# Performance work log

Measured on AMD Instinct MI355X. Metric: run time of the kernel, lower is better.

Reference implementation:

```python
import jax, jax.numpy as jnp
import numpy as np

EMB = 1024
HEADS = 16
FFN = 4096
EPS = 1e-5


def _layernorm(x, g, b):
    mu = jnp.mean(x, axis=-1, keepdims=True)
    var = jnp.mean((x - mu) ** 2, axis=-1, keepdims=True)
    return (x - mu) * jax.lax.rsqrt(var + EPS) * g + b


def setup_inputs() -> dict:
    key = jax.random.key(0)
    ks = jax.random.split(key, 8)
    B, T = 2, 2048
    s_in = 1.0 / np.sqrt(EMB)
    s_ffn = 1.0 / np.sqrt(FFN)
    return {
        "x": jax.random.normal(ks[0], (B, T, EMB), jnp.float32),
        "positions": jnp.arange(B * T, dtype=jnp.int64 if jax.config.jax_enable_x64 else jnp.int32).reshape(B, T),
        "ln1_g": jnp.ones((EMB,), jnp.float32),
        "ln1_b": jnp.zeros((EMB,), jnp.float32),
        "ln2_g": jnp.ones((EMB,), jnp.float32),
        "ln2_b": jnp.zeros((EMB,), jnp.float32),
        "Wq": jax.random.normal(ks[1], (EMB, EMB), jnp.float32) * s_in,
        "bq": jnp.zeros((EMB,), jnp.float32),
        "Wk": jax.random.normal(ks[2], (EMB, EMB), jnp.float32) * s_in,
        "bk": jnp.zeros((EMB,), jnp.float32),
        "Wv": jax.random.normal(ks[3], (EMB, EMB), jnp.float32) * s_in,
        "bv": jnp.zeros((EMB,), jnp.float32),
        "Wo": jax.random.normal(ks[4], (EMB, EMB), jnp.float32) * s_in,
        "bo": jnp.zeros((EMB,), jnp.float32),
        "W1": jax.random.normal(ks[5], (EMB, FFN), jnp.float32) * s_in,
        "b1": jnp.zeros((FFN,), jnp.float32),
        "W2": jax.random.normal(ks[6], (FFN, EMB), jnp.float32) * s_ffn,
        "b2": jnp.zeros((EMB,), jnp.float32),
    }


def reference(x, positions, ln1_g, ln1_b, ln2_g, ln2_b,
              Wq, bq, Wk, bk, Wv, bv, Wo, bo, W1, b1, W2, b2):
    B, T, C = x.shape
    H, D = HEADS, C // HEADS
    # x = ln1(x); then residual branches add onto the normalized x (as in source)
    x = _layernorm(x, ln1_g, ln1_b)
    # --- self attention (rope=None, mask=None, dropout inactive) ---
    q = (x @ Wq + bq).reshape(B, T, H, D).transpose(0, 2, 1, 3)  # [B,H,T,D]
    k = (x @ Wk + bk).reshape(B, T, H, D).transpose(0, 2, 1, 3)
    v = (x @ Wv + bv).reshape(B, T, H, D).transpose(0, 2, 1, 3)
    scale = 1.0 / jnp.sqrt(jnp.asarray(D, x.dtype))
    attn = jnp.einsum("bhtd,bhsd->bhts", q, k) * scale  # [B,H,T,T]
    attn = jax.nn.softmax(attn, axis=-1)
    attn_out = jnp.einsum("bhts,bhsd->bhtd", attn, v)
    attn_out = attn_out.transpose(0, 2, 1, 3).reshape(B, T, C)
    attn_out = attn_out @ Wo + bo
    x = x + attn_out
    # --- FFN with exact (erf) GELU, matching torch nn.GELU default ---
    h = _layernorm(x, ln2_g, ln2_b)
    h = jax.nn.gelu(h @ W1 + b1, approximate=False)
    h = h @ W2 + b2
    return x + h
```

## Files before the change

kernel.cpp:

```cpp
#include <hip/hip_runtime.h>
#include <cstdint>
#include <cstddef>

typedef __bf16 bf16;
typedef __bf16 bf16x8 __attribute__((ext_vector_type(8)));
typedef __bf16 bf16x4 __attribute__((ext_vector_type(4)));
typedef float f32x4 __attribute__((ext_vector_type(4)));
typedef float f32x16 __attribute__((ext_vector_type(16)));

#define TOKENS 4096
#define TSEQ   2048
#define NHEADS 16
#define HDIM   64
#define CDIM   1024

typedef __attribute__((address_space(3))) unsigned int lds_uint;
typedef __attribute__((address_space(1))) const unsigned int g_uint;
__device__ __forceinline__ void glds16(const bf16* g, bf16* l) {
  __builtin_amdgcn_global_load_lds((g_uint*)g, (lds_uint*)l, 16, 0, 0);
}

__device__ __forceinline__ float gelu_f(float v) {
  float g2 = v * (1.5957691216f + 0.0713548163f * v * v);
  return v / (1.0f + __expf(-g2));
}

#define NBUF 17
struct DetectArgs { const void* p[NBUF]; int n[NBUF]; };

__global__ __launch_bounds__(256) void detect_kernel(DetectArgs a, int* __restrict__ flags) {
  __shared__ int s_nz, s_bl;
  if (threadIdx.x == 0) { s_nz = 0; s_bl = 0; }
  __syncthreads();
  int i = blockIdx.x;
  const unsigned int* w = (const unsigned int*)a.p[i];
  int nwords = a.n[i] / 2; if (nwords > 2048) nwords = 2048;
  int nz = 0, bl = 0;
  for (int j = threadIdx.x; j < nwords; j += 256) {
    unsigned int v = w[j];
    if (v != 0u) {
      nz++;
      unsigned int e = (v >> 7) & 0xFFu;
      if (e >= 100u && e <= 140u) bl++;
    }
  }
  atomicAdd(&s_nz, nz);
  atomicAdd(&s_bl, bl);
  __syncthreads();
  if (threadIdx.x == 0) flags[i] = (2 * s_bl >= s_nz) ? 1 : 0;
}

__device__ __forceinline__ float ld_any(const void* p, size_t idx, bool isb) {
  return isb ? (float)((const bf16*)p)[idx] : ((const float*)p)[idx];
}

__device__ __forceinline__ void ln_stats(float s, float s2, int tid, float& mu, float& rstd) {
#pragma unroll
  for (int off = 32; off; off >>= 1) {
    s  += __shfl_down(s, off);
    s2 += __shfl_down(s2, off);
  }
  __shared__ float red[8];
  int w = tid >> 6;
  if ((tid & 63) == 0) { red[w] = s; red[4 + w] = s2; }
  __syncthreads();
  if (tid == 0) {
    red[0] = red[0] + red[1] + red[2] + red[3];
    red[4] = red[4] + red[5] + red[6] + red[7];
  }
  __syncthreads();
  mu = red[0] * (1.0f / CDIM);
  float var = fmaxf(red[4] * (1.0f / CDIM) - mu * mu, 0.f);
  rstd = rsqrtf(var + 1e-5f);
}

__global__ __launch_bounds__(256) void ln_f32(const float* __restrict__ x,
                                              const bf16* __restrict__ g,
                                              const bf16* __restrict__ b,
                                              bf16* __restrict__ y) {
  int row = blockIdx.x, tid = threadIdx.x;
  float v[4]; float s = 0.f, s2 = 0.f;
#pragma unroll
  for (int i = 0; i < 4; i++) {
    float f = x[(size_t)row * CDIM + tid * 4 + i];
    v[i] = f; s += f; s2 += f * f;
  }
  float mu, rstd;
  ln_stats(s, s2, tid, mu, rstd);
  bf16* yr = y + (size_t)row * CDIM;
#pragma unroll
  for (int i = 0; i < 4; i++) {
    int c = tid * 4 + i;
    yr[c] = (bf16)((v[i] - mu) * rstd * (float)g[c] + (float)b[c]);
  }
}

struct MegaArgs {
  const void* w_in[6]; bf16* w_out[6]; int wK[6], wN[6], wflag[6];
  const void* vp[10]; bf16* vd[10]; int vn[10], vfi[10];
  const void* x; const void* graw; const void* braw; bf16* y;
};

__global__ __launch_bounds__(256) void mega_pre(MegaArgs a, const int* __restrict__ flags) {
  int bid = blockIdx.x;
  int tx = threadIdx.x, ty = threadIdx.y;
  int tid = tx + ty * 64;
  if (bid < 3072) {
    __shared__ bf16 tile[64][65];
    int mi, start;
    if (bid < 1024)      { mi = bid >> 8; start = mi << 8; }
    else if (bid < 2048) { mi = 4; start = 1024; }
    else                 { mi = 5; start = 2048; }
    int tb = bid - start;
    int nT = a.wN[mi] >> 6;
    int kb = (tb / nT) * 64, nb = (tb % nT) * 64;
    int K = a.wK[mi], N = a.wN[mi];
    bool isb = flags[a.wflag[mi]] != 0;
    const void* in = a.w_in[mi]; bf16* out = a.w_out[mi];
    for (int i = ty; i < 64; i += 4)
      tile[i][tx] = (bf16)ld_any(in, (size_t)(kb + i) * N + nb + tx, isb);
    __syncthreads();
    for (int i = ty; i < 64; i += 4)
      out[(size_t)(nb + i) * K + kb + tx] = tile[tx][i];
  } else if (bid == 3072) {
    for (int i = 0; i < 10; i++) {
      bool isb = flags[a.vfi[i]] != 0;
      const void* in = a.vp[i]; bf16* out = a.vd[i]; int n = a.vn[i];
      for (int j = tid; j < n; j += 256)
        out[j] = (bf16)ld_any(in, j, isb);
    }
  } else {
    int row = bid - 3073;
    bool isb  = flags[0] != 0;
    bool gisb = flags[1] != 0;
    bool bisb = flags[2] != 0;
    float v[4]; float s = 0.f, s2 = 0.f;
#pragma unroll
    for (int i = 0; i < 4; i++) {
      float f = ld_any(a.x, (size_t)row * CDIM + tid * 4 + i, isb);
      v[i] = f; s += f; s2 += f * f;
    }
    float mu, rstd;
    ln_stats(s, s2, tid, mu, rstd);
    bf16* yr = a.y + (size_t)row * CDIM;
#pragma unroll
    for (int i = 0; i < 4; i++) {
      int c = tid * 4 + i;
      float gv = ld_any(a.graw, c, gisb);
      float bv = ld_any(a.braw, c, bisb);
      yr[c] = (bf16)((v[i] - mu) * rstd * gv + bv);
    }
  }
}

template <int BM, int BN>
__device__ __forceinline__ void gemm_core(const bf16* __restrict__ A,
                                          const bf16* __restrict__ Bt,
                                          int K, int m0, int n0,
                                          bf16* As, bf16* Bs,
                                          f32x4 (&acc)[BM / 32][BN / 32]) {
  constexpr int SI = BM / 32, SJ = BN / 32;
  int t = threadIdx.x;
  int wave = t >> 6, lane = t & 63, quad = lane >> 4, l16 = lane & 15;
  int wm = (wave & 1) * (BM / 2), wn = (wave >> 1) * (BN / 2);
  int srow = t >> 2, sc = t & 3;
  int swz = (srow >> 1) & 3;
  const bf16* ga[BM / 64];
  const bf16* gb[BN / 64];
#pragma unroll
  for (int h = 0; h < BM / 64; h++)
    ga[h] = A + (size_t)(m0 + h * 64 + srow) * K + (sc ^ swz) * 8;
#pragma unroll
  for (int h = 0; h < BN / 64; h++)
    gb[h] = Bt + (size_t)(n0 + h * 64 + srow) * K + (sc ^ swz) * 8;

  for (int k0 = 0; k0 < K; k0 += 64) {
#pragma unroll
    for (int q = 0; q < 2; q++) {
#pragma unroll
      for (int h = 0; h < BM / 64; h++)
        glds16(ga[h] + k0 + q * 32, As + q * (BM * 32) + h * 2048 + srow * 32 + sc * 8);
#pragma unroll
      for (int h = 0; h < BN / 64; h++)
        glds16(gb[h] + k0 + q * 32, Bs + q * (BN * 32) + h * 2048 + srow * 32 + sc * 8);
    }
    __syncthreads();
#pragma unroll
    for (int q = 0; q < 2; q++) {
      bf16x8 af[SI], bfr[SJ];
#pragma unroll
      for (int i = 0; i < SI; i++) {
        int m = wm + i * 16 + l16;
        af[i] = *(const bf16x8*)&As[q * (BM * 32) + m * 32 + ((quad ^ ((m >> 1) & 3)) * 8)];
      }
#pragma unroll
      for (int j = 0; j < SJ; j++) {
        int n = wn + j * 16 + l16;
        bfr[j] = *(const bf16x8*)&Bs[q * (BN * 32) + n * 32 + ((quad ^ ((n >> 1) & 3)) * 8)];
      }
#pragma unroll
      for (int i = 0; i < SI; i++)
#pragma unroll
        for (int j = 0; j < SJ; j++)
          acc[i][j] = __builtin_amdgcn_mfma_f32_16x16x32_bf16(af[i], bfr[j], acc[i][j], 0, 0, 0);
    }
    __syncthreads();
  }
}

#define EPI_NONE 0
#define EPI_RES  1
#define EPI_GELU 2

template <int BM, int BN, int EPI, typename OutT, typename ResT>
__global__ __launch_bounds__(256) void gemm128(const bf16* __restrict__ A,
                                               const bf16* __restrict__ Bt,
                                               const bf16* __restrict__ bias,
                                               const ResT* __restrict__ res,
                                               OutT* __restrict__ C,
                                               int N, int K) {
  __shared__ alignas(16) bf16 As[2 * BM * 32];
  __shared__ alignas(16) bf16 Bs[2 * BN * 32];
  int m0 = blockIdx.y * BM, n0 = blockIdx.x * BN;
  f32x4 acc[BM / 32][BN / 32] = {};
  gemm_core<BM, BN>(A, Bt, K, m0, n0, As, Bs, acc);

  int t = threadIdx.x, wave = t >> 6, lane = t & 63, quad = lane >> 4, l16 = lane & 15;
  int wm = (wave & 1) * (BM / 2), wn = (wave >> 1) * (BN / 2);
#pragma unroll
  for (int i = 0; i < BM / 32; i++)
#pragma unroll
    for (int j = 0; j < BN / 32; j++) {
      int n = n0 + wn + j * 16 + l16;
      float bv = (float)bias[n];
#pragma unroll
      for (int r = 0; r < 4; r++) {
        int m = m0 + wm + i * 16 + quad * 4 + r;
        float v = acc[i][j][r] + bv;
        if (EPI == EPI_GELU)      v = gelu_f(v);
        else if (EPI == EPI_RES)  v += (float)res[(size_t)m * N + n];
        C[(size_t)m * N + n] = (OutT)v;
      }
    }
}

__device__ __forceinline__ void gemm256_core(const bf16* __restrict__ A,
                                             const bf16* __restrict__ Bt,
                                             int K, int m0, int n0,
                                             bf16* sm, f32x4 (&acc)[8][4]) {
  const int NT = K >> 6;
  const int t = threadIdx.x;
  const int lane = t & 63, quad = lane >> 4, l16 = lane & 15;
  const int wave = t >> 6;
  const int wm = (wave & 1) * 128, wn = (wave >> 1) * 64;
  const int srow = t >> 2, sc = t & 3;
  const int swz = (srow >> 1) & 3;
  const int rA = (srow & 63) + ((srow >> 6) << 7);
  const bf16* gA = A + (size_t)(m0 + rA) * K + ((sc ^ swz) << 3);
  const bf16* gB = Bt + (size_t)(n0 + srow) * K + ((sc ^ swz) << 3);
  const int ldsA = rA * 32 + sc * 8;
  const int ldsB = srow * 32 + sc * 8;

  auto stA = [&](int tile, int u) {
    if (tile >= NT) return;
    const bf16* g = gA + (size_t)(u << 6) * K + (tile << 6);
    bf16* l = sm + ((tile & 1) << 15) + ldsA + (u << 11);
    glds16(g, l);
    glds16(g + 32, l + 8192);
  };
  auto stB = [&](int tile, int h) {
    if (tile >= NT) return;
    const bf16* g = gB + (size_t)(h << 7) * K + (tile << 6);
    bf16* l = sm + ((tile & 1) << 15) + 16384 + ldsB + (h << 12);
    glds16(g, l);
    glds16(g + 32, l + 8192);
  };

  stB(0, 0); stB(0, 1); stA(0, 0); stA(0, 1);
  stB(1, 0); stB(1, 1); stA(1, 0);
  asm volatile("s_waitcnt vmcnt(6)" ::: "memory");
  __builtin_amdgcn_s_barrier();
  asm volatile("" ::: "memory");

  bf16x8 bfr[2][4];

#define LDB256(buf)                                                        \
  _Pragma("unroll") for (int q = 0; q < 2; q++)                            \
  _Pragma("unroll") for (int j = 0; j < 4; j++) {                          \
    int nl = wn + j * 16 + l16;                                            \
    bfr[q][j] = *(const bf16x8*)&sm[((buf) << 15) + 16384 + q * 8192 +     \
                                    nl * 32 + ((quad ^ ((nl >> 1) & 3)) << 3)]; \
  }

#define PHASE256(buf, P, STAGE, EXTRAWAIT)                                 \
  {                                                                        \
    bf16x8 af[2][2];                                                       \
    _Pragma("unroll") for (int q = 0; q < 2; q++)                          \
    _Pragma("unroll") for (int i2 = 0; i2 < 2; i2++) {                     \
      int ml = wm + (P) * 32 + i2 * 16 + l16;                              \
      af[q][i2] = *(const bf16x8*)&sm[((buf) << 15) + q * 8192 + ml * 32 + \
                                      ((quad ^ ((ml >> 1) & 3)) << 3)];    \
    }                                                                      \
    if ((P) == 0) { LDB256(buf); }                                         \
    STAGE;                                                                 \
    asm volatile("" ::: "memory");                                         \
    __builtin_amdgcn_s_barrier();                                          \
    asm volatile("s_waitcnt lgkmcnt(0)" ::: "memory");                     \
    __builtin_amdgcn_s_setprio(1);                                         \
    _Pragma("unroll") for (int q = 0; q < 2; q++)                          \
    _Pragma("unroll") for (int i2 = 0; i2 < 2; i2++)                       \
    _Pragma("unroll") for (int j = 0; j < 4; j++)                          \
      acc[(P) * 2 + i2][j] = __builtin_amdgcn_mfma_f32_16x16x32_bf16(      \
          af[q][i2], bfr[q][j], acc[(P) * 2 + i2][j], 0, 0, 0);            \
    __builtin_amdgcn_s_setprio(0);                                         \
    asm volatile("" ::: "memory");                                         \
    EXTRAWAIT;                                                             \
    __builtin_amdgcn_s_barrier();                                          \
    asm volatile("" ::: "memory");                                         \
  }

  for (int t0 = 0; t0 < NT; t0 += 2) {
    const int t1 = t0 + 1;
    PHASE256(0, 0, stA(t1, 1), (void)0);
    PHASE256(0, 1, stB(t0 + 2, 0), (void)0);
    PHASE256(0, 2, stB(t0 + 2, 1), (void)0);
    PHASE256(0, 3, stA(t0 + 2, 0),
             asm volatile("s_waitcnt vmcnt(6)" ::: "memory"));
    PHASE256(1, 0, stA(t0 + 2, 1), (void)0);
    PHASE256(1, 1, stB(t1 + 2, 0), (void)0);
    PHASE256(1, 2, stB(t1 + 2, 1), (void)0);
    PHASE256(1, 3, stA(t1 + 2, 0),
             asm volatile("s_waitcnt vmcnt(6)" ::: "memory"));
  }
#undef PHASE256
#undef LDB256
}

__device__ __forceinline__ void xcd_swizzle(int& bx, int& by) {
  int gx = gridDim.x;
  int nwg = gx * gridDim.y;
  int bid = blockIdx.x + blockIdx.y * gx;
  int wg = (bid & 7) * (nwg >> 3) + (bid >> 3);
  bx = wg % gx; by = wg / gx;
}

__global__ __launch_bounds__(512, 2) void gemm256_gelu(const bf16* __restrict__ A,
                                                       const bf16* __restrict__ Bt,
                                                       const bf16* __restrict__ bias,
                                                       bf16* __restrict__ C,
                                                       int N, int K) {
  __shared__ alignas(16) bf16 sm[65536];
  int bx, by; xcd_swizzle(bx, by);
  int m0 = by * 256, n0 = bx * 256;
  f32x4 acc[8][4] = {};
  gemm256_core(A, Bt, K, m0, n0, sm, acc);

  int t = threadIdx.x, wave = t >> 6, lane = t & 63, quad = lane >> 4, l16 = lane & 15;
  int wm = (wave & 1) * 128, wn = (wave >> 1) * 64;
#pragma unroll
  for (int i = 0; i < 8; i++)
#pragma unroll
    for (int j = 0; j < 4; j++) {
      int n = n0 + wn + j * 16 + l16;
      float bv = (float)bias[n];
#pragma unroll
      for (int r = 0; r < 4; r++) {
        int m = m0 + wm + i * 16 + quad * 4 + r;
        C[(size_t)m * N + n] = (bf16)gelu_f(acc[i][j][r] + bv);
      }
    }
}

__global__ __launch_bounds__(512, 2) void gemm256_qkv(const bf16* __restrict__ A,
                                                      const bf16* __restrict__ Bt,
                                                      const bf16* __restrict__ bias,
                                                      bf16* __restrict__ QK,
                                                      bf16* __restrict__ Vt) {
  __shared__ alignas(16) bf16 sm[65536];
  int bx, by; xcd_swizzle(bx, by);
  int m0 = by * 256, n0 = bx * 256;
  f32x4 acc[8][4] = {};
  gemm256_core(A, Bt, 1024, m0, n0, sm, acc);

  int t = threadIdx.x, wave = t >> 6, lane = t & 63, quad = lane >> 4, l16 = lane & 15;
  int wm = (wave & 1) * 128, wn = (wave >> 1) * 64;
#pragma unroll
  for (int i = 0; i < 8; i++)
#pragma unroll
    for (int j = 0; j < 4; j++) {
      int n = n0 + wn + j * 16 + l16;
      float bv = (float)bias[n];
      int mb = m0 + wm + i * 16 + quad * 4;
      if (n < 1024) {
#pragma unroll
        for (int r = 0; r < 4; r++)
          QK[(size_t)(mb + r) * 2048 + n] = (bf16)((acc[i][j][r] + bv) * 0.18033688011112042f);
      } else if (n < 2048) {
#pragma unroll
        for (int r = 0; r < 4; r++)
          QK[(size_t)(mb + r) * 2048 + n] = (bf16)(acc[i][j][r] + bv);
      } else {
        bf16x4 pk;
#pragma unroll
        for (int r = 0; r < 4; r++) pk[r] = (bf16)(acc[i][j][r] + bv);
        *(bf16x4*)&Vt[(size_t)(n - 2048) * TOKENS + mb] = pk;
      }
    }
}

__global__ __launch_bounds__(256, 2) void attn_kernel(const bf16* __restrict__ QK,
                                                      const bf16* __restrict__ Vt,
                                                      bf16* __restrict__ O) {
  __shared__ alignas(16) bf16 Ks[2][4096];
  __shared__ alignas(16) bf16 Vs[2][4096];
  __shared__ alignas(16) bf16 Ps[4][2048];
  int b = blockIdx.z, h = blockIdx.y, q0 = blockIdx.x * 128;
  int t = threadIdx.x, wave = t >> 6, lane = t & 63;
  int l31 = lane & 31, l5 = lane >> 5, l7 = lane & 7;

  const bf16* Qg = QK;
  const bf16* Kg = QK + 1024;
  const size_t bT = (size_t)b * TSEQ;
  const int h64 = h * 64;

  int sr = lane >> 3;
  int sch = l7 ^ sr;
  auto stage = [&](int tile, int buf) {
    size_t krow = bT + tile * 64 + wave * 8 + sr;
    bf16* kd = &Ks[buf][wave * 512 + lane * 8];
    glds16(&Kg[krow * 2048 + h64 + sch * 8], kd);
    glds16(&Kg[(krow + 32) * 2048 + h64 + sch * 8], kd + 2048);
    size_t vrow = (size_t)(h64 + wave * 8 + sr) * TOKENS + bT + tile * 64 + sch * 8;
    bf16* vd = &Vs[buf][wave * 512 + lane * 8];
    glds16(&Vt[vrow], vd);
    glds16(&Vt[vrow + (size_t)32 * TOKENS], vd + 2048);
  };

  bf16x8 qf[4];
  {
    size_t qrow = bT + q0 + wave * 32 + l31;
    const bf16* qp = &Qg[qrow * 2048 + h64 + l5 * 8];
#pragma unroll
    for (int ds = 0; ds < 4; ds++) qf[ds] = *(const bf16x8*)(qp + ds * 16);
  }

  bf16* PW = &Ps[wave][0];
  int qb = 4 * l5, c0 = l31 >> 3;
  int pwb[8];
#pragma unroll
  for (int kvt = 0; kvt < 2; kvt++)
#pragma unroll
    for (int r3 = 0; r3 < 4; r3++)
      pwb[kvt * 4 + r3] = (qb + r3) * 64 + (((kvt * 4 + c0) ^ (r3 + qb)) * 8) + l7;

  f32x16 accO0 = {}, accO1 = {}, accL = {};
  const bf16 one = (bf16)1.0f;
  const bf16x8 onesv = {one, one, one, one, one, one, one, one};

  stage(0, 0);
  __syncthreads();

  for (int it = 0; it < TSEQ / 64; it++) {
    int cur = it & 1;
    if (it + 1 < TSEQ / 64) stage(it + 1, cur ^ 1);

    const bf16* KsC = &Ks[cur][0];
    const bf16* VsC = &Vs[cur][0];

    f32x16 st0 = {}, st1 = {};
#pragma unroll
    for (int ds = 0; ds < 4; ds++) {
      int chs = ((ds * 2 + l5) ^ l7) * 8;
      bf16x8 k0 = *(const bf16x8*)&KsC[l31 * 64 + chs];
      bf16x8 k1 = *(const bf16x8*)&KsC[(32 + l31) * 64 + chs];
      st0 = __builtin_amdgcn_mfma_f32_32x32x16_bf16(qf[ds], k0, st0, 0, 0, 0);
      st1 = __builtin_amdgcn_mfma_f32_32x32x16_bf16(qf[ds], k1, st1, 0, 0, 0);
    }

#pragma unroll
    for (int r = 0; r < 16; r++)
      PW[pwb[r & 3] + (r >> 2) * 512] = (bf16)exp2f(fminf(st0[r], 86.f));
#pragma unroll
    for (int r = 0; r < 16; r++)
      PW[pwb[4 + (r & 3)] + (r >> 2) * 512] = (bf16)exp2f(fminf(st1[r], 86.f));

    bf16x8 pa[4];
#pragma unroll
    for (int ks = 0; ks < 4; ks++)
      pa[ks] = *(const bf16x8*)&PW[l31 * 64 + (((ks * 2 + l5) ^ l7) * 8)];

#pragma unroll
    for (int ks = 0; ks < 4; ks++) {
      int chs = ((ks * 2 + l5) ^ l7) * 8;
      bf16x8 v0 = *(const bf16x8*)&VsC[l31 * 64 + chs];
      bf16x8 v1 = *(const bf16x8*)&VsC[(32 + l31) * 64 + chs];
      accO0 = __builtin_amdgcn_mfma_f32_32x32x16_bf16(pa[ks], v0, accO0, 0, 0, 0);
      accO1 = __builtin_amdgcn_mfma_f32_32x32x16_bf16(pa[ks], v1, accO1, 0, 0, 0);
      accL  = __builtin_amdgcn_mfma_f32_32x32x16_bf16(pa[ks], onesv, accL, 0, 0, 0);
    }

    __syncthreads();
  }

#pragma unroll
  for (int r = 0; r < 16; r++) {
    int q = (r & 3) + 8 * (r >> 2) + 4 * l5;
    float rl = 1.0f / fmaxf(accL[r], 1e-30f);
    size_t orow = (bT + q0 + wave * 32 + q) * CDIM + h64;
    O[orow + l31]      = (bf16)(accO0[r] * rl);
    O[orow + 32 + l31] = (bf16)(accO1[r] * rl);
  }
}

extern "C" void kernel_launch(void* const* d_in, const int* in_sizes, int n_in,
                              void* d_out, int out_size, void* d_ws, size_t ws_size,
                              hipStream_t stream) {
  char* ws = (char*)d_ws;
  const size_t MB = 1024 * 1024;
  const size_t KB = 1024;

  int* flags = (int*)ws;
  bf16* vec_c = (bf16*)(ws + 4 * KB);
  bf16* ln1g_c = vec_c + 0 * 8192;
  bf16* ln1b_c = vec_c + 1 * 8192;
  bf16* ln2g_c = vec_c + 2 * 8192;
  bf16* ln2b_c = vec_c + 3 * 8192;
  bf16* bqkv_c = vec_c + 4 * 8192;
  bf16* bo_c   = vec_c + 6 * 8192;
  bf16* b1_c   = vec_c + 7 * 8192;
  bf16* b2_c   = vec_c + 8 * 8192;

  bf16*  WqkvT  = (bf16*)(ws + 1 * MB);
  bf16*  WoT    = (bf16*)(ws + 7 * MB);
  bf16*  W1T    = (bf16*)(ws + 9 * MB);
  bf16*  W2T    = (bf16*)(ws + 17 * MB);
  bf16*  xn     = (bf16*)(ws + 25 * MB);
  bf16*  QKbuf  = (bf16*)(ws + 33 * MB);
  bf16*  Vtbuf  = (bf16*)(ws + 49 * MB);
  bf16*  ab     = (bf16*)(ws + 57 * MB);
  float* xmid32 = (float*)(ws + 65 * MB);
  bf16*  h2     = (bf16*)(ws + 81 * MB);
  bf16*  f1     = (bf16*)(ws + 33 * MB);

  const int din_idx[NBUF] = {0, 2, 3, 4, 5, 6, 7, 8, 9, 10, 11, 12, 13, 14, 15, 16, 17};
  DetectArgs da;
  for (int i = 0; i < NBUF; i++) { da.p[i] = d_in[din_idx[i]]; da.n[i] = in_sizes[din_idx[i]]; }
  detect_kernel<<<NBUF, 256, 0, stream>>>(da, flags);

  MegaArgs ma;
  {
    const void* wi[6] = {d_in[6], d_in[8], d_in[10], d_in[12], d_in[14], d_in[16]};
    bf16* wo[6] = {WqkvT, WqkvT + 1024 * 1024, WqkvT + 2 * 1024 * 1024, WoT, W1T, W2T};
    const int wK[6] = {1024, 1024, 1024, 1024, 1024, 4096};
    const int wN[6] = {1024, 1024, 1024, 1024, 4096, 1024};
    const int wf[6] = {5, 7, 9, 11, 13, 15};
    for (int i = 0; i < 6; i++) {
      ma.w_in[i] = wi[i]; ma.w_out[i] = wo[i];
      ma.wK[i] = wK[i]; ma.wN[i] = wN[i]; ma.wflag[i] = wf[i];
    }
    const int vf[10] = {1, 2, 3, 4, 6, 8, 10, 12, 14, 16};
    bf16* vd[10] = {ln1g_c, ln1b_c, ln2g_c, ln2b_c,
                    bqkv_c, bqkv_c + 1024, bqkv_c + 2048, bo_c, b1_c, b2_c};
    for (int i = 0; i < 10; i++) {
      int di = din_idx[vf[i]];
      ma.vp[i] = d_in[di]; ma.vd[i] = vd[i]; ma.vn[i] = in_sizes[di]; ma.vfi[i] = vf[i];
    }
    ma.x = d_in[0]; ma.graw = d_in[2]; ma.braw = d_in[3]; ma.y = xn;
  }
  mega_pre<<<3072 + 1 + TOKENS, dim3(64, 4), 0, stream>>>(ma, flags);

  gemm256_qkv<<<dim3(12, 16), 512, 0, stream>>>(xn, WqkvT, bqkv_c, QKbuf, Vtbuf);

  attn_kernel<<<dim3(TSEQ / 128, NHEADS, 2), 256, 0, stream>>>(QKbuf, Vtbuf, ab);

  gemm128<64, 128, EPI_RES, float, bf16><<<dim3(8, 64), 256, 0, stream>>>(
      ab, WoT, bo_c, xn, xmid32, 1024, 1024);

  ln_f32<<<TOKENS, 256, 0, stream>>>(xmid32, ln2g_c, ln2b_c, h2);

  gemm256_gelu<<<dim3(16, 16), 512, 0, stream>>>(h2, W1T, b1_c, f1, 4096, 1024);

  gemm128<64, 128, EPI_RES, float, float><<<dim3(8, 64), 256, 0, stream>>>(
      f1, W2T, b2_c, xmid32, (float*)d_out, 1024, 4096);
}
```

Before: 395.4 us.

## Keep attention probabilities in registers via transposed QK^T and remap blocks per XCD

The attention kernel now computes S^T (K as the A operand, Q as B), so each lane's score accumulator already sits in the layout the PV MFMA needs as its A operand. Probabilities are exponentiated straight into registers, which removes the per-wave LDS round trip for P and its shared buffer. V fragments are rebuilt from two 4-element LDS reads to match the new operand layout. Separately, the launch becomes a 1-D grid with a swizzle that places all query tiles of a (batch, head) on the same XCD, aiming for better L2 reuse of K/V. The trade-off is more, narrower LDS reads for V.

```diff
diff --git a/kernel.cpp b/kernel.cpp
--- a/kernel.cpp
+++ b/kernel.cpp
@@ -413,8 +413,11 @@
                                                       bf16* __restrict__ O) {
   __shared__ alignas(16) bf16 Ks[2][4096];
   __shared__ alignas(16) bf16 Vs[2][4096];
-  __shared__ alignas(16) bf16 Ps[4][2048];
-  int b = blockIdx.z, h = blockIdx.y, q0 = blockIdx.x * 128;
+  int bid = blockIdx.x;
+  int xcd = bid & 7, slot = bid >> 3;
+  int g = xcd + 8 * (slot >> 4);
+  int q0 = (slot & 15) * 128;
+  int h = g & 15, b = g >> 4;
   int t = threadIdx.x, wave = t >> 6, lane = t & 63;
   int l31 = lane & 31, l5 = lane >> 5, l7 = lane & 7;
 
@@ -444,18 +447,16 @@
     for (int ds = 0; ds < 4; ds++) qf[ds] = *(const bf16x8*)(qp + ds * 16);
   }
 
-  bf16* PW = &Ps[wave][0];
-  int qb = 4 * l5, c0 = l31 >> 3;
-  int pwb[8];
-#pragma unroll
-  for (int kvt = 0; kvt < 2; kvt++)
-#pragma unroll
-    for (int r3 = 0; r3 < 4; r3++)
-      pwb[kvt * 4 + r3] = (qb + r3) * 64 + (((kvt * 4 + c0) ^ (r3 + qb)) * 8) + l7;
-
   f32x16 accO0 = {}, accO1 = {}, accL = {};
   const bf16 one = (bf16)1.0f;
   const bf16x8 onesv = {one, one, one, one, one, one, one, one};
+
+  auto vread = [&](const bf16* VsC, int d, int w) -> bf16x8 {
+    union { struct { bf16x4 lo, hi; } p; bf16x8 v; } u;
+    u.p.lo = *(const bf16x4*)&VsC[d * 64 + (((2 * w) ^ l7) * 8) + 4 * l5];
+    u.p.hi = *(const bf16x4*)&VsC[d * 64 + (((2 * w + 1) ^ l7) * 8) + 4 * l5];
+    return u.v;
+  };
 
   stage(0, 0);
   __syncthreads();
@@ -473,30 +474,26 @@
       int chs = ((ds * 2 + l5) ^ l7) * 8;
       bf16x8 k0 = *(const bf16x8*)&KsC[l31 * 64 + chs];
       bf16x8 k1 = *(const bf16x8*)&KsC[(32 + l31) * 64 + chs];
-      st0 = __builtin_amdgcn_mfma_f32_32x32x16_bf16(qf[ds], k0, st0, 0, 0, 0);
-      st1 = __builtin_amdgcn_mfma_f32_32x32x16_bf16(qf[ds], k1, st1, 0, 0, 0);
-    }
-
-#pragma unroll
-    for (int r = 0; r < 16; r++)
-      PW[pwb[r & 3] + (r >> 2) * 512] = (bf16)exp2f(fminf(st0[r], 86.f));
-#pragma unroll
-    for (int r = 0; r < 16; r++)
-      PW[pwb[4 + (r & 3)] + (r >> 2) * 512] = (bf16)exp2f(fminf(st1[r], 86.f));
+      st0 = __builtin_amdgcn_mfma_f32_32x32x16_bf16(k0, qf[ds], st0, 0, 0, 0);
+      st1 = __builtin_amdgcn_mfma_f32_32x32x16_bf16(k1, qf[ds], st1, 0, 0, 0);
+    }
 
     bf16x8 pa[4];
 #pragma unroll
-    for (int ks = 0; ks < 4; ks++)
-      pa[ks] = *(const bf16x8*)&PW[l31 * 64 + (((ks * 2 + l5) ^ l7) * 8)];
-
-#pragma unroll
-    for (int ks = 0; ks < 4; ks++) {
-      int chs = ((ks * 2 + l5) ^ l7) * 8;
-      bf16x8 v0 = *(const bf16x8*)&VsC[l31 * 64 + chs];
-      bf16x8 v1 = *(const bf16x8*)&VsC[(32 + l31) * 64 + chs];
-      accO0 = __builtin_amdgcn_mfma_f32_32x32x16_bf16(pa[ks], v0, accO0, 0, 0, 0);
-      accO1 = __builtin_amdgcn_mfma_f32_32x32x16_bf16(pa[ks], v1, accO1, 0, 0, 0);
-      accL  = __builtin_amdgcn_mfma_f32_32x32x16_bf16(pa[ks], onesv, accL, 0, 0, 0);
+    for (int j = 0; j < 8; j++) {
+      pa[0][j] = (bf16)exp2f(fminf(st0[j], 86.f));
+      pa[1][j] = (bf16)exp2f(fminf(st0[8 + j], 86.f));
+      pa[2][j] = (bf16)exp2f(fminf(st1[j], 86.f));
+      pa[3][j] = (bf16)exp2f(fminf(st1[8 + j], 86.f));
+    }
+
+#pragma unroll
+    for (int w = 0; w < 4; w++) {
+      bf16x8 v0 = vread(VsC, l31, w);
+      bf16x8 v1 = vread(VsC, 32 + l31, w);
+      accO0 = __builtin_amdgcn_mfma_f32_32x32x16_bf16(pa[w], v0, accO0, 0, 0, 0);
+      accO1 = __builtin_amdgcn_mfma_f32_32x32x16_bf16(pa[w], v1, accO1, 0, 0, 0);
+      accL  = __builtin_amdgcn_mfma_f32_32x32x16_bf16(pa[w], onesv, accL, 0, 0, 0);
     }
 
     __syncthreads();
@@ -571,7 +568,7 @@
 
   gemm256_qkv<<<dim3(12, 16), 512, 0, stream>>>(xn, WqkvT, bqkv_c, QKbuf, Vtbuf);
 
-  attn_kernel<<<dim3(TSEQ / 128, NHEADS, 2), 256, 0, stream>>>(QKbuf, Vtbuf, ab);
+  attn_kernel<<<512, 256, 0, stream>>>(QKbuf, Vtbuf, ab);
 
   gemm128<64, 128, EPI_RES, float, bf16><<<dim3(8, 64), 256, 0, stream>>>(
       ab, WoT, bo_c, xn, xmid32, 1024, 1024);
```

Result: no change. 393.1 us (-0.6%).
